# Performance work log

Hardware: AMD Instinct MI355X
Metric: run time of the kernel (lower is better)

The kernel has to match this reference:

```python
import jax, jax.numpy as jnp
import numpy as np

IN_DIM = 512
OUT_DIM = 512
DEGREE = 3
KNOTS = (0.2, 0.4, 0.6, 0.8)
SDIM = DEGREE + 1 + len(KNOTS)  # 8
BATCH = 2048


def truncated_power_basis(t):
    # t: (B,) -> (B, SDIM)
    cols = [jnp.ones_like(t)]
    for p in range(1, DEGREE + 1):
        cols.append(t ** p)
    for c in KNOTS:  # degree > 1 branch: relu(t - knot)^degree
        cols.append(jax.nn.relu(t - c) ** DEGREE)
    return jnp.stack(cols, axis=1)


def setup_inputs() -> dict:
    key = jax.random.key(0)
    k0, k1, k2 = jax.random.split(key, 3)
    inputs = jax.random.uniform(k0, (BATCH, IN_DIM + 1), dtype=jnp.float32)
    # xavier_uniform for W_wts (fan_in=SDIM, fan_out=IN_DIM*OUT_DIM)
    limW = float(np.sqrt(6.0 / (SDIM + IN_DIM * OUT_DIM)))
    W_wts = jax.random.uniform(k1, (SDIM, IN_DIM * OUT_DIM), dtype=jnp.float32,
                               minval=-limW, maxval=limW)
    limb = float(np.sqrt(6.0 / (SDIM + OUT_DIM)))
    b_wts = jax.random.uniform(k2, (SDIM, OUT_DIM), dtype=jnp.float32,
                               minval=-limb, maxval=limb)
    return {"inputs": inputs, "W_wts": W_wts, "b_wts": b_wts}


def reference(inputs, W_wts, b_wts):
    treatment = inputs[:, 0]          # (B,)
    features = inputs[:, 1:]          # (B, IN_DIM)
    basis = truncated_power_basis(treatment)  # (B, SDIM)
    Wk = W_wts.reshape(SDIM, IN_DIM, OUT_DIM)
    # fused: per-sample weight W[b] = sum_s basis[b,s] * Wk[s]; out[b] = features[b] @ W[b]
    out = jnp.einsum('bs,bi,sio->bo', basis, features, Wk)
    out = out + basis @ b_wts         # (B, OUT_DIM)
    return out
```

## Files before the change

kernel.cpp:

```cpp
#include <hip/hip_runtime.h>
#include <stdint.h>

#define BATCH   2048
#define INDIM   512
#define OUTDIM  512
#define SDIM    8
#define KTOT    4096
#define SPLITK  8

typedef __attribute__((ext_vector_type(4))) float  f32x4;
typedef __attribute__((ext_vector_type(8))) __bf16 bf16x8;
typedef __attribute__((ext_vector_type(8))) unsigned short u16x8;

__device__ __forceinline__ unsigned short f2bf(float x) {
  unsigned int u = __float_as_uint(x);
  u += 0x7fffu + ((u >> 16) & 1u);
  return (unsigned short)(u >> 16);
}

__device__ __forceinline__ void llds16(const void* g, void* s) {
  __builtin_amdgcn_global_load_lds(
      (__attribute__((address_space(1))) void*)g,
      (__attribute__((address_space(3))) void*)s, 16, 0, 0);
}

__device__ __forceinline__ void mkbasis(float t, float* bs) {
  bs[0] = 1.0f; bs[1] = t; bs[2] = t * t; bs[3] = bs[2] * t;
  const float kn[4] = {0.2f, 0.4f, 0.6f, 0.8f};
#pragma unroll
  for (int c = 0; c < 4; ++c) {
    float d = fmaxf(t - kn[c], 0.0f);
    bs[4 + c] = d * d * d;
  }
}

__global__ __launch_bounds__(256) void prep_kernel(
    const float* __restrict__ inp, const float* __restrict__ W,
    const float* __restrict__ bwts, unsigned short* __restrict__ Fbf,
    unsigned short* __restrict__ Btf, float* __restrict__ Bas,
    float* __restrict__ out) {
  const int tid = threadIdx.x;
  const int bx  = blockIdx.x;
  if (bx < 512) {
    const int kt = bx >> 3, ntile = bx & 7;
    const int k0 = kt * 64, n0 = ntile * 64;
    __shared__ float Ts[64][65];
#pragma unroll
    for (int p = 0; p < 4; ++p) {
      const int r  = (tid >> 4) + p * 16;
      const int c4 = (tid & 15) * 4;
      float4 v = *(const float4*)&W[(size_t)(k0 + r) * 512 + n0 + c4];
      Ts[c4 + 0][r] = v.x; Ts[c4 + 1][r] = v.y;
      Ts[c4 + 2][r] = v.z; Ts[c4 + 3][r] = v.w;
    }
    __syncthreads();
    const int nl  = tid >> 2;
    const int kcc = (tid & 3) * 16;
    u16x8 o0, o1;
#pragma unroll
    for (int q = 0; q < 8; ++q) {
      o0[q] = f2bf(Ts[nl][kcc + q]);
      o1[q] = f2bf(Ts[nl][kcc + 8 + q]);
    }
    unsigned short* dst = Btf + (size_t)(n0 + nl) * KTOT + k0 + kcc;
    *(u16x8*)dst = o0;
    *(u16x8*)(dst + 8) = o1;
  } else if (bx < 1024) {
    const int b0   = (bx - 512) * 4;
    const int b    = b0 + (tid >> 6);
    const int i0   = (tid & 63) * 8;
    const float* row = inp + (size_t)b * (INDIM + 1);
    u16x8 o;
#pragma unroll
    for (int q = 0; q < 8; ++q) o[q] = f2bf(row[1 + i0 + q]);
    *(u16x8*)(Fbf + (size_t)b * INDIM + i0) = o;
    if (tid < 4) {
      const int bb = b0 + tid;
      float t = inp[(size_t)bb * (INDIM + 1)];
      float bs[8]; mkbasis(t, bs);
      f32x4 lo = {bs[0], bs[1], bs[2], bs[3]};
      f32x4 hi = {bs[4], bs[5], bs[6], bs[7]};
      *(f32x4*)(Bas + (size_t)bb * 8)     = lo;
      *(f32x4*)(Bas + (size_t)bb * 8 + 4) = hi;
    }
  } else {
    const int bb = (bx - 1024) * 2 + (tid >> 7);
    const int o0 = (tid & 127) * 4;
    float t = inp[(size_t)bb * (INDIM + 1)];
    float bs[8]; mkbasis(t, bs);
    float4 a = make_float4(0.f, 0.f, 0.f, 0.f);
#pragma unroll
    for (int s = 0; s < 8; ++s) {
      float4 wv = *(const float4*)&bwts[s * OUTDIM + o0];
      a.x += bs[s] * wv.x; a.y += bs[s] * wv.y;
      a.z += bs[s] * wv.z; a.w += bs[s] * wv.w;
    }
    *(float4*)&out[(size_t)bb * OUTDIM + o0] = a;
  }
}

__global__ __launch_bounds__(256, 2) void gemm_kernel(
    const unsigned short* __restrict__ Fbf,
    const unsigned short* __restrict__ Btf,
    const float* __restrict__ Bas,
    float* __restrict__ out) {
  const int tid  = threadIdx.x;
  const int s    = blockIdx.x & (SPLITK - 1);
  const int tile = blockIdx.x >> 3;
  const int nt = tile & 3, mt = tile >> 2;
  const int m0 = mt * 128, n0 = nt * 128;
  const int l = tid & 63, w = tid >> 6;
  const int wm = w >> 1, wn = w & 1;
  const int quad = l >> 4, lr = l & 15;

  __shared__ __align__(16) unsigned short As[128 * 64];
  __shared__ __align__(16) unsigned short Bs[128 * 64];

  f32x4 acc[4][4] = {};

  const int sr = tid >> 3, pc = tid & 7;
  const int lc = pc ^ (sr & 7);
  const unsigned short* Ag = Fbf + (size_t)(m0 + sr) * INDIM + lc * 8;
  const unsigned short* Bg = Btf + (size_t)(n0 + sr) * KTOT + (size_t)s * 512 + lc * 8;

  const int sx = lr & 7;
  const int c0 = (quad ^ sx) * 8;
  const int c1 = ((4 + quad) ^ sx) * 8;
  int arow[4], brow[4];
#pragma unroll
  for (int i = 0; i < 4; ++i) {
    arow[i] = (wm * 64 + i * 16 + lr) * 64;
    brow[i] = (wn * 64 + i * 16 + lr) * 64;
  }

  for (int it = 0; it < 8; ++it) {
    const int koff = it * 64;
#pragma unroll
    for (int j = 0; j < 4; ++j) {
      llds16(Ag + koff + (size_t)(j * 32) * INDIM, &As[j * 2048 + tid * 8]);
      llds16(Bg + koff + (size_t)(j * 32) * KTOT,  &Bs[j * 2048 + tid * 8]);
    }
    __syncthreads();

    bf16x8 a0[4], a1[4], b0[4], b1[4];
#pragma unroll
    for (int i = 0; i < 4; ++i) {
      a0[i] = *(const bf16x8*)&As[arow[i] + c0];
      a1[i] = *(const bf16x8*)&As[arow[i] + c1];
      b0[i] = *(const bf16x8*)&Bs[brow[i] + c0];
      b1[i] = *(const bf16x8*)&Bs[brow[i] + c1];
    }
#pragma unroll
    for (int i = 0; i < 4; ++i)
#pragma unroll
      for (int j = 0; j < 4; ++j) {
        acc[i][j] = __builtin_amdgcn_mfma_f32_16x16x32_bf16(a0[i], b0[j], acc[i][j], 0, 0, 0);
        acc[i][j] = __builtin_amdgcn_mfma_f32_16x16x32_bf16(a1[i], b1[j], acc[i][j], 0, 0, 0);
      }
    __syncthreads();
  }

  float bsv[4][4];
#pragma unroll
  for (int i = 0; i < 4; ++i) {
    const int rowb = m0 + wm * 64 + i * 16 + quad * 4;
#pragma unroll
    for (int r = 0; r < 4; ++r)
      bsv[i][r] = Bas[(size_t)(rowb + r) * 8 + s];
  }
#pragma unroll
  for (int i = 0; i < 4; ++i) {
    const int rowb = m0 + wm * 64 + i * 16 + quad * 4;
#pragma unroll
    for (int j = 0; j < 4; ++j) {
      const int col = n0 + wn * 64 + j * 16 + lr;
      float* o = out + (size_t)rowb * OUTDIM + col;
#pragma unroll
      for (int r = 0; r < 4; ++r)
        unsafeAtomicAdd(o + (size_t)r * OUTDIM, acc[i][j][r] * bsv[i][r]);
    }
  }
}

extern "C" void kernel_launch(void* const* d_in, const int* in_sizes, int n_in,
                              void* d_out, int out_size, void* d_ws, size_t ws_size,
                              hipStream_t stream) {
  const float* inp  = (const float*)d_in[0];
  const float* W    = (const float*)d_in[1];
  const float* bwts = (const float*)d_in[2];
  float* out = (float*)d_out;

  unsigned short* Fbf = (unsigned short*)d_ws;
  unsigned short* Btf = Fbf + (size_t)BATCH * INDIM;
  float*          Bas = (float*)(Btf + (size_t)OUTDIM * KTOT);

  prep_kernel<<<2048, 256, 0, stream>>>(inp, W, bwts, Fbf, Btf, Bas, out);
  gemm_kernel<<<(BATCH / 128) * (OUTDIM / 128) * SPLITK, 256, 0, stream>>>(Fbf, Btf, Bas, out);
}
```

Measured before the change: 102.4 us.

## Replace split-K atomics with in-block basis reduction and fused bias epilogue

The GEMM no longer uses 8 split-K blocks that atomically add scaled partials into the output. Each 512-thread block now owns a 64x64 output tile. Its 8 waves each handle one basis slice, reading B fragments straight from global memory and A from a fully LDS-resident feature tile. The per-wave partials are reduced through LDS with the basis weights and the bias term added in, then written with plain stores, so the separate bias prep blocks and the atomics go away. The cost is one large LDS footprint, which limits occupancy, and B loads that are not staged through LDS.

```diff
diff --git a/kernel.cpp b/kernel.cpp
--- a/kernel.cpp
+++ b/kernel.cpp
@@ -6,7 +6,8 @@
 #define OUTDIM  512
 #define SDIM    8
 #define KTOT    4096
-#define SPLITK  8
+#define PSTRIDE 68
+#define PSZ     (64 * PSTRIDE)
 
 typedef __attribute__((ext_vector_type(4))) float  f32x4;
 typedef __attribute__((ext_vector_type(8))) __bf16 bf16x8;
@@ -36,9 +37,8 @@
 
 __global__ __launch_bounds__(256) void prep_kernel(
     const float* __restrict__ inp, const float* __restrict__ W,
-    const float* __restrict__ bwts, unsigned short* __restrict__ Fbf,
-    unsigned short* __restrict__ Btf, float* __restrict__ Bas,
-    float* __restrict__ out) {
+    unsigned short* __restrict__ Fbf, unsigned short* __restrict__ Btf,
+    float* __restrict__ Bas) {
   const int tid = threadIdx.x;
   const int bx  = blockIdx.x;
   if (bx < 512) {
@@ -65,7 +65,7 @@
     unsigned short* dst = Btf + (size_t)(n0 + nl) * KTOT + k0 + kcc;
     *(u16x8*)dst = o0;
     *(u16x8*)(dst + 8) = o1;
-  } else if (bx < 1024) {
+  } else {
     const int b0   = (bx - 512) * 4;
     const int b    = b0 + (tid >> 6);
     const int i0   = (tid & 63) * 8;
@@ -83,103 +83,90 @@
       *(f32x4*)(Bas + (size_t)bb * 8)     = lo;
       *(f32x4*)(Bas + (size_t)bb * 8 + 4) = hi;
     }
-  } else {
-    const int bb = (bx - 1024) * 2 + (tid >> 7);
-    const int o0 = (tid & 127) * 4;
-    float t = inp[(size_t)bb * (INDIM + 1)];
-    float bs[8]; mkbasis(t, bs);
-    float4 a = make_float4(0.f, 0.f, 0.f, 0.f);
-#pragma unroll
-    for (int s = 0; s < 8; ++s) {
-      float4 wv = *(const float4*)&bwts[s * OUTDIM + o0];
-      a.x += bs[s] * wv.x; a.y += bs[s] * wv.y;
-      a.z += bs[s] * wv.z; a.w += bs[s] * wv.w;
-    }
-    *(float4*)&out[(size_t)bb * OUTDIM + o0] = a;
   }
 }
 
-__global__ __launch_bounds__(256, 2) void gemm_kernel(
+__global__ __launch_bounds__(512, 2) void gemm_kernel(
     const unsigned short* __restrict__ Fbf,
     const unsigned short* __restrict__ Btf,
     const float* __restrict__ Bas,
+    const float* __restrict__ bwts,
     float* __restrict__ out) {
   const int tid  = threadIdx.x;
-  const int s    = blockIdx.x & (SPLITK - 1);
-  const int tile = blockIdx.x >> 3;
-  const int nt = tile & 3, mt = tile >> 2;
-  const int m0 = mt * 128, n0 = nt * 128;
-  const int l = tid & 63, w = tid >> 6;
-  const int wm = w >> 1, wn = w & 1;
+  const int tile = blockIdx.x;
+  const int nt = tile & 7, mt = tile >> 3;
+  const int m0 = mt * 64, n0 = nt * 64;
+  const int w = tid >> 6;
+  const int l = tid & 63;
   const int quad = l >> 4, lr = l & 15;
 
-  __shared__ __align__(16) unsigned short As[128 * 64];
-  __shared__ __align__(16) unsigned short Bs[128 * 64];
+  __shared__ __align__(16) float smem[8 * PSZ];
+  unsigned short* Alds = (unsigned short*)smem;
 
+#pragma unroll
+  for (int j = 0; j < 8; ++j) {
+    const int f   = j * 512 + tid;
+    const int row = f >> 6;
+    const int cs  = (f & 63) ^ (row & 7);
+    llds16(Fbf + (size_t)(m0 + row) * INDIM + cs * 8, &Alds[f * 8]);
+  }
+  __syncthreads();
+
+  const unsigned short* bptr[4];
+#pragma unroll
+  for (int j = 0; j < 4; ++j)
+    bptr[j] = Btf + (size_t)(n0 + j * 16 + lr) * KTOT + w * 512 + quad * 8;
+
+  const int sx = lr & 7;
   f32x4 acc[4][4] = {};
 
-  const int sr = tid >> 3, pc = tid & 7;
-  const int lc = pc ^ (sr & 7);
-  const unsigned short* Ag = Fbf + (size_t)(m0 + sr) * INDIM + lc * 8;
-  const unsigned short* Bg = Btf + (size_t)(n0 + sr) * KTOT + (size_t)s * 512 + lc * 8;
-
-  const int sx = lr & 7;
-  const int c0 = (quad ^ sx) * 8;
-  const int c1 = ((4 + quad) ^ sx) * 8;
-  int arow[4], brow[4];
+#pragma unroll 4
+  for (int ks = 0; ks < 16; ++ks) {
+    bf16x8 bfr[4], afr[4];
 #pragma unroll
-  for (int i = 0; i < 4; ++i) {
-    arow[i] = (wm * 64 + i * 16 + lr) * 64;
-    brow[i] = (wn * 64 + i * 16 + lr) * 64;
-  }
-
-  for (int it = 0; it < 8; ++it) {
-    const int koff = it * 64;
+    for (int j = 0; j < 4; ++j)
+      bfr[j] = *(const bf16x8*)(bptr[j] + ks * 32);
+    const int c = ((ks * 4 + quad) ^ sx) * 8;
 #pragma unroll
-    for (int j = 0; j < 4; ++j) {
-      llds16(Ag + koff + (size_t)(j * 32) * INDIM, &As[j * 2048 + tid * 8]);
-      llds16(Bg + koff + (size_t)(j * 32) * KTOT,  &Bs[j * 2048 + tid * 8]);
-    }
-    __syncthreads();
-
-    bf16x8 a0[4], a1[4], b0[4], b1[4];
-#pragma unroll
-    for (int i = 0; i < 4; ++i) {
-      a0[i] = *(const bf16x8*)&As[arow[i] + c0];
-      a1[i] = *(const bf16x8*)&As[arow[i] + c1];
-      b0[i] = *(const bf16x8*)&Bs[brow[i] + c0];
-      b1[i] = *(const bf16x8*)&Bs[brow[i] + c1];
-    }
+    for (int i = 0; i < 4; ++i)
+      afr[i] = *(const bf16x8*)&Alds[(i * 16 + lr) * 512 + c];
 #pragma unroll
     for (int i = 0; i < 4; ++i)
 #pragma unroll
-      for (int j = 0; j < 4; ++j) {
-        acc[i][j] = __builtin_amdgcn_mfma_f32_16x16x32_bf16(a0[i], b0[j], acc[i][j], 0, 0, 0);
-        acc[i][j] = __builtin_amdgcn_mfma_f32_16x16x32_bf16(a1[i], b1[j], acc[i][j], 0, 0, 0);
-      }
-    __syncthreads();
+      for (int j = 0; j < 4; ++j)
+        acc[i][j] = __builtin_amdgcn_mfma_f32_16x16x32_bf16(afr[i], bfr[j], acc[i][j], 0, 0, 0);
   }
 
-  float bsv[4][4];
+  __syncthreads();
+
+  float* P = smem + w * PSZ;
 #pragma unroll
-  for (int i = 0; i < 4; ++i) {
-    const int rowb = m0 + wm * 64 + i * 16 + quad * 4;
+  for (int i = 0; i < 4; ++i)
 #pragma unroll
-    for (int r = 0; r < 4; ++r)
-      bsv[i][r] = Bas[(size_t)(rowb + r) * 8 + s];
-  }
-#pragma unroll
-  for (int i = 0; i < 4; ++i) {
-    const int rowb = m0 + wm * 64 + i * 16 + quad * 4;
-#pragma unroll
-    for (int j = 0; j < 4; ++j) {
-      const int col = n0 + wn * 64 + j * 16 + lr;
-      float* o = out + (size_t)rowb * OUTDIM + col;
+    for (int j = 0; j < 4; ++j)
 #pragma unroll
       for (int r = 0; r < 4; ++r)
-        unsafeAtomicAdd(o + (size_t)r * OUTDIM, acc[i][j][r] * bsv[i][r]);
-    }
+        P[(i * 16 + quad * 4 + r) * PSTRIDE + j * 16 + lr] = acc[i][j][r];
+
+  __syncthreads();
+
+  const int row  = tid >> 3;
+  const int col8 = (tid & 7) * 8;
+  const float* brow = Bas + (size_t)(m0 + row) * 8;
+  f32x4 s0 = {}, s1 = {};
+#pragma unroll
+  for (int ww = 0; ww < 8; ++ww) {
+    const float bw = brow[ww];
+    const float* Pr = smem + ww * PSZ + row * PSTRIDE + col8;
+    const float* Wr = bwts + (size_t)ww * OUTDIM + n0 + col8;
+    f32x4 v0 = *(const f32x4*)Pr + *(const f32x4*)Wr;
+    f32x4 v1 = *(const f32x4*)(Pr + 4) + *(const f32x4*)(Wr + 4);
+    s0 += v0 * bw;
+    s1 += v1 * bw;
   }
+  float* op = out + (size_t)(m0 + row) * OUTDIM + n0 + col8;
+  *(f32x4*)op       = s0;
+  *(f32x4*)(op + 4) = s1;
 }
 
 extern "C" void kernel_launch(void* const* d_in, const int* in_sizes, int n_in,
@@ -194,6 +181,6 @@
   unsigned short* Btf = Fbf + (size_t)BATCH * INDIM;
   float*          Bas = (float*)(Btf + (size_t)OUTDIM * KTOT);
 
-  prep_kernel<<<2048, 256, 0, stream>>>(inp, W, bwts, Fbf, Btf, Bas, out);
-  gemm_kernel<<<(BATCH / 128) * (OUTDIM / 128) * SPLITK, 256, 0, stream>>>(Fbf, Btf, Bas, out);
+  prep_kernel<<<1024, 256, 0, stream>>>(inp, W, Fbf, Btf, Bas);
+  gemm_kernel<<<(BATCH / 64) * (OUTDIM / 64), 512, 0, stream>>>(Fbf, Btf, Bas, bwts, out);
 }
```

Result: faster. 87.32 us (-14.7%).
